# Kernel tuning notes

Measured on AMD Instinct MI355X. Metric: run time of the kernel, lower is better.

Reference implementation:

```python
import jax, jax.numpy as jnp
import numpy as np

B, T, C, H = 2, 2048, 1024, 16
D = C // H
EPS = 1e-5

def _layer_norm(x, w, b):
    mu = jnp.mean(x, axis=-1, keepdims=True)
    var = jnp.var(x, axis=-1, keepdims=True)
    return (x - mu) * jax.lax.rsqrt(var + EPS) * w + b

def setup_inputs() -> dict:
    key = jax.random.key(0)
    ks = jax.random.split(key, 8)
    s = 0.02
    return {
        "x": jax.random.normal(ks[0], (B, T, C), jnp.float32),
        "ln1_w": jnp.ones((C,), jnp.float32),
        "ln1_b": jnp.zeros((C,), jnp.float32),
        "wq": jax.random.normal(ks[1], (C, C), jnp.float32) * s,
        "bq": jnp.zeros((C,), jnp.float32),
        "wk": jax.random.normal(ks[2], (C, C), jnp.float32) * s,
        "bk": jnp.zeros((C,), jnp.float32),
        "wv": jax.random.normal(ks[3], (C, C), jnp.float32) * s,
        "bv": jnp.zeros((C,), jnp.float32),
        "wo": jax.random.normal(ks[4], (C, C), jnp.float32) * s,
        "bo": jnp.zeros((C,), jnp.float32),
        "ln2_w": jnp.ones((C,), jnp.float32),
        "ln2_b": jnp.zeros((C,), jnp.float32),
        "w1": jax.random.normal(ks[5], (C, 4 * C), jnp.float32) * s,
        "b1": jnp.zeros((4 * C,), jnp.float32),
        "w2": jax.random.normal(ks[6], (4 * C, C), jnp.float32) * s,
        "b2": jnp.zeros((C,), jnp.float32),
    }

def reference(x, ln1_w, ln1_b, wq, bq, wk, bk, wv, bv, wo, bo,
              ln2_w, ln2_b, w1, b1, w2, b2):
    # --- attention branch ---
    h = _layer_norm(x, ln1_w, ln1_b)
    q = (h @ wq + bq).reshape(B, T, H, D).transpose(0, 2, 1, 3)  # [B,H,T,D]
    k = (h @ wk + bk).reshape(B, T, H, D).transpose(0, 2, 1, 3)
    v = (h @ wv + bv).reshape(B, T, H, D).transpose(0, 2, 1, 3)
    att = jnp.einsum("bhqd,bhkd->bhqk", q, k) * (1.0 / np.sqrt(D))
    causal = jnp.tril(jnp.ones((T, T), dtype=bool))
    att = jnp.where(causal[None, None], att, jnp.float32(-jnp.inf))
    att = jax.nn.softmax(att, axis=-1)
    y = jnp.einsum("bhqk,bhkd->bhqd", att, v)
    y = y.transpose(0, 2, 1, 3).reshape(B, T, C)
    y = y @ wo + bo
    x = x + y
    # --- MLP branch ---
    h = _layer_norm(x, ln2_w, ln2_b)
    h = jax.nn.gelu(h @ w1 + b1, approximate=False)
    h = h @ w2 + b2
    return x + h
```

## Files before the change

### kernel.cpp

```cpp
#include <hip/hip_runtime.h>
#include <hip/hip_bf16.h>
#include <math.h>

#define B_  2
#define T_  2048
#define C_  1024
#define H_  16
#define D_  64
#define BT_ (B_*T_)

typedef __hip_bfloat16 bf16;
typedef short bf16x8 __attribute__((ext_vector_type(8)));
typedef float floatx4 __attribute__((ext_vector_type(4)));

struct alignas(8) bf4 { bf16 v[4]; };

#define GLOAD_LDS16(g, l) __builtin_amdgcn_global_load_lds(            \
    (const __attribute__((address_space(1))) void*)(g),                \
    (__attribute__((address_space(3))) void*)(l), 16, 0, 0)

__global__ __launch_bounds__(256) void ln_bf16_kernel(const float* __restrict__ x,
    const float* __restrict__ w, const float* __restrict__ b,
    bf16* __restrict__ out)
{
    __shared__ float ps[4], ps2[4];
    __shared__ float sm, srs;
    const int row = blockIdx.x;
    const int tid = threadIdx.x;
    float4 v = ((const float4*)(x + (size_t)row * C_))[tid];
    float s  = v.x + v.y + v.z + v.w;
    float s2 = v.x*v.x + v.y*v.y + v.z*v.z + v.w*v.w;
    for (int off = 32; off > 0; off >>= 1) {
        s  += __shfl_down(s,  off);
        s2 += __shfl_down(s2, off);
    }
    const int wid = tid >> 6;
    if ((tid & 63) == 0) { ps[wid] = s; ps2[wid] = s2; }
    __syncthreads();
    if (tid == 0) {
        float ts  = ps[0] + ps[1] + ps[2] + ps[3];
        float ts2 = ps2[0] + ps2[1] + ps2[2] + ps2[3];
        float mean = ts * (1.0f / C_);
        float var  = ts2 * (1.0f / C_) - mean * mean;
        sm  = mean;
        srs = rsqrtf(var + 1e-5f);
    }
    __syncthreads();
    const float mean = sm, rs = srs;
    float4 wv = ((const float4*)w)[tid];
    float4 bv = ((const float4*)b)[tid];
    bf4 o;
    o.v[0] = __float2bfloat16((v.x - mean) * rs * wv.x + bv.x);
    o.v[1] = __float2bfloat16((v.y - mean) * rs * wv.y + bv.y);
    o.v[2] = __float2bfloat16((v.z - mean) * rs * wv.z + bv.z);
    o.v[3] = __float2bfloat16((v.w - mean) * rs * wv.w + bv.w);
    *(bf4*)(out + (size_t)row * C_ + tid * 4) = o;
}

__device__ __forceinline__ void wconv_body(const float* __restrict__ W,
    bf16* __restrict__ Wt, int K, int N, int k0, int n0)
{
    __shared__ float L[64][65];
    const int t = threadIdx.x;
    const int r = t >> 4, c4 = t & 15;
    #pragma unroll
    for (int p = 0; p < 4; ++p) {
        const int kr = p * 16 + r;
        const float4 v = *(const float4*)(W + (size_t)(k0 + kr) * N + n0 + c4 * 4);
        L[kr][c4*4+0] = v.x; L[kr][c4*4+1] = v.y;
        L[kr][c4*4+2] = v.z; L[kr][c4*4+3] = v.w;
    }
    __syncthreads();
    #pragma unroll
    for (int p = 0; p < 4; ++p) {
        const int nr = p * 16 + r;
        bf4 o;
        o.v[0] = __float2bfloat16(L[c4*4+0][nr]);
        o.v[1] = __float2bfloat16(L[c4*4+1][nr]);
        o.v[2] = __float2bfloat16(L[c4*4+2][nr]);
        o.v[3] = __float2bfloat16(L[c4*4+3][nr]);
        *(bf4*)(Wt + (size_t)(n0 + nr) * K + k0 + c4 * 4) = o;
    }
}

__global__ __launch_bounds__(256) void wconv4_kernel(
    const float* __restrict__ wq, const float* __restrict__ wk,
    const float* __restrict__ wv, const float* __restrict__ wo,
    bf16* __restrict__ wqkvT, bf16* __restrict__ woT)
{
    const int z = blockIdx.z;
    const float* W = (z == 0) ? wq : (z == 1) ? wk : (z == 2) ? wv : wo;
    bf16* Wt = (z == 3) ? woT : wqkvT + (size_t)z * 1024 * 1024;
    wconv_body(W, Wt, 1024, 1024, blockIdx.x * 64, blockIdx.y * 64);
}

__global__ __launch_bounds__(256) void wconv2_kernel(
    const float* __restrict__ w1, const float* __restrict__ w2,
    bf16* __restrict__ w1T, bf16* __restrict__ w2T)
{
    if (blockIdx.z == 0)
        wconv_body(w1, w1T, 1024, 4096, blockIdx.x * 64, blockIdx.y * 64);
    else
        wconv_body(w2, w2T, 4096, 1024, blockIdx.y * 64, blockIdx.x * 64);
}

__global__ void bcat_kernel(const float* __restrict__ bq, const float* __restrict__ bk,
                            const float* __restrict__ bv, float* __restrict__ o)
{
    const int i = blockIdx.x * 256 + threadIdx.x;
    float v = (i < 1024) ? bq[i] : (i < 2048 ? bk[i - 1024] : bv[i - 2048]);
    o[i] = v;
}

__global__ __launch_bounds__(256) void splitk_reduce_kernel(
    float* __restrict__ out, const float* __restrict__ p1,
    const float* __restrict__ bias, const float* __restrict__ res)
{
    const size_t i = (size_t)blockIdx.x * 256 + threadIdx.x;
    float4 o = ((const float4*)out)[i];
    const float4 p = ((const float4*)p1)[i];
    const float4 bb = ((const float4*)bias)[i & (C_ / 4 - 1)];
    const float4 xx = ((const float4*)res)[i];
    o.x += p.x + bb.x + xx.x;
    o.y += p.y + bb.y + xx.y;
    o.z += p.z + bb.z + xx.z;
    o.w += p.w + bb.w + xx.w;
    ((float4*)out)[i] = o;
}

template<int TM, int TN, int BK>
__global__ __launch_bounds__(256) void mfma_gemm_t(
    const bf16* __restrict__ A, const bf16* __restrict__ Wt,
    const float* __restrict__ bias, const float* __restrict__ res,
    void* __restrict__ outv, bf16* __restrict__ vT, float* __restrict__ psplit,
    int M, int N, int K, int ldk, int mode)
{
    constexpr int MI = TM / 32;
    constexpr int NJ = TN / 32;
    constexpr int CPR = BK / 8;
    constexpr int NSLOT = (TM + TN) * CPR / 256;
    __shared__ __align__(16) bf16 smem[(TM + TN) * BK];
    bf16* As = smem;
    bf16* Bs = smem + TM * BK;
    const int tid = threadIdx.x;
    const int w = tid >> 6, l = tid & 63;
    const int fm = l & 15, qd = l >> 4;
    const int m0 = blockIdx.x * TM, n0 = blockIdx.y * TN;
    const int bz = blockIdx.z;
    const int wr = (w >> 1) * (TM / 2), wc = (w & 1) * (TN / 2);

    const bf16* Ab = A  + (size_t)bz * K;
    const bf16* Wb = Wt + (size_t)bz * K;

    const bf16* gsrc[NSLOT];
    bf16* ldst[NSLOT];
    #pragma unroll
    for (int p = 0; p < NSLOT; ++p) {
        const int s = tid + p * 256;
        if (s < TM * CPR) {
            const int row = s / CPR, pos = s % CPR;
            const int ch = pos ^ (row & (CPR - 1));
            gsrc[p] = Ab + (size_t)(m0 + row) * ldk + ch * 8;
            ldst[p] = As + s * 8;
        } else {
            const int s2 = s - TM * CPR;
            const int row = s2 / CPR, pos = s2 % CPR;
            const int ch = pos ^ (row & (CPR - 1));
            gsrc[p] = Wb + (size_t)(n0 + row) * ldk + ch * 8;
            ldst[p] = Bs + s2 * 8;
        }
    }

    floatx4 acc[MI][NJ] = {};

    const int nk = K / BK;
    for (int kk = 0; kk < nk; ++kk) {
        const size_t ko = (size_t)kk * BK;
        __syncthreads();
        #pragma unroll
        for (int p = 0; p < NSLOT; ++p)
            GLOAD_LDS16(gsrc[p] + ko, ldst[p]);
        __syncthreads();
        #pragma unroll
        for (int ks = 0; ks < BK / 32; ++ks) {
            bf16x8 af[MI], bfr[NJ];
            #pragma unroll
            for (int i = 0; i < MI; ++i) {
                const int row = wr + i * 16 + fm;
                af[i] = *(const bf16x8*)(As + row * BK
                        + (((ks * 4 + qd) ^ (row & (CPR - 1))) * 8));
            }
            #pragma unroll
            for (int j = 0; j < NJ; ++j) {
                const int row = wc + j * 16 + fm;
                bfr[j] = *(const bf16x8*)(Bs + row * BK
                        + (((ks * 4 + qd) ^ (row & (CPR - 1))) * 8));
            }
            #pragma unroll
            for (int i = 0; i < MI; ++i)
                #pragma unroll
                for (int j = 0; j < NJ; ++j)
                    acc[i][j] = __builtin_amdgcn_mfma_f32_16x16x32_bf16(
                        af[i], bfr[j], acc[i][j], 0, 0, 0);
        }
    }

    const int col0 = n0 + wc;
    const int row0 = m0 + wr;
    const bool isv = (mode == 3) && (col0 >= 2048);
    const bool bounce = (mode == 0) || (mode == 1) || (mode == 3 && !isv);
    __syncthreads();

    if (bounce) {
        constexpr int RM = TM / 2, RN = TN / 2, CHN = RN / 8;
        bf16* eb = smem + w * (RM * RN);
        #pragma unroll
        for (int j = 0; j < NJ; ++j) {
            const int col = col0 + j * 16 + fm;
            const float bb = bias[col];
            const bool isq = (mode == 3) && (col0 + j * 16 < 1024);
            const int lc = j * 16 + fm;
            #pragma unroll
            for (int i = 0; i < MI; ++i) {
                floatx4 a = acc[i][j];
                #pragma unroll
                for (int r = 0; r < 4; ++r) {
                    float vv = a[r] + bb;
                    if (mode == 1) {
                        float zz = vv * (0.7978845608f + 0.0356774081f * vv * vv);
                        zz = fminf(zz, 15.0f);
                        const float e = __expf(2.0f * zz);
                        vv = vv * (e / (e + 1.0f));
                    }
                    if (isq) vv *= 0.125f;
                    const int lr = i * 16 + qd * 4 + r;
                    const int pch = ((lc >> 3) + 2 * qd) & (CHN - 1);
                    eb[lr * RN + pch * 8 + (lc & 7)] = __float2bfloat16(vv);
                }
            }
        }
        bf16* o = (bf16*)outv;
        #pragma unroll
        for (int c = 0; c < RM * RN / 512; ++c) {
            const int idx = c * 64 + l;
            const int row = idx / CHN;
            const int c8  = idx % CHN;
            const int pch = (c8 + 2 * ((row >> 2) & 3)) & (CHN - 1);
            const bf16x8 vv = *(const bf16x8*)(eb + row * RN + pch * 8);
            *(bf16x8*)(o + (size_t)(row0 + row) * N + col0 + c8 * 8) = vv;
        }
    } else {
        #pragma unroll
        for (int j = 0; j < NJ; ++j) {
            const int col = col0 + j * 16 + fm;
            const float bb = bias[col];
            #pragma unroll
            for (int i = 0; i < MI; ++i) {
                const int row = row0 + i * 16 + qd * 4;
                floatx4 a = acc[i][j];
                if (mode == 4) {
                    float* o = bz ? psplit : (float*)outv;
                    #pragma unroll
                    for (int r = 0; r < 4; ++r)
                        o[(size_t)(row + r) * N + col] = a[r];
                } else if (mode == 2) {
                    float* o = (float*)outv;
                    #pragma unroll
                    for (int r = 0; r < 4; ++r)
                        o[(size_t)(row + r) * N + col] =
                            a[r] + bb + res[(size_t)(row + r) * N + col];
                } else {
                    bf4 pv;
                    #pragma unroll
                    for (int r = 0; r < 4; ++r) pv.v[r] = __float2bfloat16(a[r] + bb);
                    *(bf4*)(vT + (size_t)(col - 2048) * M + row) = pv;
                }
            }
        }
    }
}


#define G8_BARRIER() do {                                   \
    __builtin_amdgcn_sched_barrier(0);                      \
    asm volatile("" ::: "memory");                          \
    __builtin_amdgcn_s_barrier();                           \
    asm volatile("" ::: "memory");                          \
    __builtin_amdgcn_sched_barrier(0);                      \
  } while (0)

#define G8_WAIT_LGKM0() do {                                        \
    asm volatile("s_waitcnt lgkmcnt(0)" ::: "memory");              \
    __builtin_amdgcn_sched_barrier(0);                              \
  } while (0)

#define G8_WAIT_VM(n) asm volatile("s_waitcnt vmcnt(" #n ")" ::: "memory")

#define G8_VW2() do { if (st1) G8_WAIT_VM(8); else G8_WAIT_VM(2); } while (0)
#define G8_VW3() do { if (st1) G8_WAIT_VM(8); else G8_WAIT_VM(0); } while (0)
#define G8_VW1() do { if (st2) G8_WAIT_VM(8); else if (st1) G8_WAIT_VM(4); \
                      else G8_WAIT_VM(0); } while (0)

#define G8_PHASE(Aq, Bq, SC, SG, DB, KO, VW)                                   \
  do {                                                                         \
    const bf16* pa0 = smem + cur * BUF + aof0 + (Aq) * 8192;                   \
    const bf16* pa1 = smem + cur * BUF + aof1 + (Aq) * 8192;                   \
    const bf16* pb0 = smem + cur * BUF + bof0 + (Bq) * 2048;                   \
    const bf16* pb1 = smem + cur * BUF + bof1 + (Bq) * 2048;                   \
    bf16x8 af[4][2], bv[2][2];                                                 \
    _Pragma("unroll")                                                          \
    for (int i = 0; i < 4; ++i) {                                              \
      af[i][0] = *(const bf16x8*)(pa0 + i * 1024);                             \
      af[i][1] = *(const bf16x8*)(pa1 + i * 1024);                             \
    }                                                                          \
    _Pragma("unroll")                                                          \
    for (int jj = 0; jj < 2; ++jj) {                                           \
      bv[jj][0] = *(const bf16x8*)(pb0 + jj * 1024);                           \
      bv[jj][1] = *(const bf16x8*)(pb1 + jj * 1024);                           \
    }                                                                          \
    if (SC) {                                                                  \
      GLOAD_LDS16(gsrc[(SG)*2]     + (KO), smem + (DB) * BUF + lof[(SG)*2]);   \
      GLOAD_LDS16(gsrc[(SG)*2 + 1] + (KO), smem + (DB) * BUF + lof[(SG)*2+1]); \
    }                                                                          \
    G8_BARRIER();                                                              \
    G8_WAIT_LGKM0();                                                           \
    __builtin_amdgcn_s_setprio(1);                                             \
    _Pragma("unroll")                                                          \
    for (int i = 0; i < 4; ++i)                                                \
      _Pragma("unroll")                                                        \
      for (int jj = 0; jj < 2; ++jj) {                                         \
        acc[(Aq)*4+i][(Bq)*2+jj] = __builtin_amdgcn_mfma_f32_16x16x32_bf16(    \
            af[i][0], bv[jj][0], acc[(Aq)*4+i][(Bq)*2+jj], 0, 0, 0);           \
        acc[(Aq)*4+i][(Bq)*2+jj] = __builtin_amdgcn_mfma_f32_16x16x32_bf16(    \
            af[i][1], bv[jj][1], acc[(Aq)*4+i][(Bq)*2+jj], 0, 0, 0);           \
      }                                                                        \
    __builtin_amdgcn_s_setprio(0);                                             \
    VW;                                                                        \
    G8_BARRIER();                                                              \
  } while (0)

template<int MODE>
__global__ __launch_bounds__(512, 2) void gemm8_t(
    const bf16* __restrict__ A, const bf16* __restrict__ Wt,
    const float* __restrict__ bias, bf16* __restrict__ out,
    bf16* __restrict__ vT, int M, int N, int K)
{
    constexpr int BUF = 32768;
    __shared__ __align__(16) bf16 smem[2 * BUF];

    const int tid = threadIdx.x;
    const int w = tid >> 6, l = tid & 63;
    const int fm = l & 15, qd = l >> 4;
    const int wm = w >> 2, wn = w & 3;

    const int nbx = gridDim.x;
    const int nwg = nbx * gridDim.y;
    const int bid = blockIdx.y * nbx + blockIdx.x;
    const int cpx = nwg >> 3;
    const int swz = (bid & 7) * cpx + (bid >> 3);
    const int m0 = (swz % nbx) * 256;
    const int n0 = (swz / nbx) * 256;

    const bf16* gsrc[8];
    int lof[8];
    #pragma unroll
    for (int g = 0; g < 4; ++g) {
        const int isB  = (g & 1);
        const int half = (g >> 1);
        #pragma unroll
        for (int s = 0; s < 2; ++s) {
            const int c = tid + s * 512;
            const int pos = c & 7;
            int row, lofe;
            const bf16* gb;
            if (!isB) {
                row  = half * 128 + (c >> 3);
                gb   = A + (size_t)(m0 + row) * K;
                lofe = row * 64 + pos * 8;
            } else {
                const int vr = c >> 3;
                row  = (vr >> 5) * 64 + half * 32 + (vr & 31);
                gb   = Wt + (size_t)(n0 + row) * K;
                lofe = 16384 + row * 64 + pos * 8;
            }
            const int ch = pos ^ (row & 7);
            gsrc[g * 2 + s] = gb + ch * 8;
            lof[g * 2 + s]  = lofe;
        }
    }

    const int sw0 = qd ^ (fm & 7);
    const int aof0 = (wm * 64 + fm) * 64 + sw0 * 8;
    const int aof1 = (wm * 64 + fm) * 64 + (sw0 ^ 4) * 8;
    const int bof0 = 16384 + (wn * 64 + fm) * 64 + sw0 * 8;
    const int bof1 = 16384 + (wn * 64 + fm) * 64 + (sw0 ^ 4) * 8;

    floatx4 acc[8][4] = {};

    #pragma unroll
    for (int s2 = 0; s2 < 8; ++s2)
        GLOAD_LDS16(gsrc[s2], smem + lof[s2]);
    GLOAD_LDS16(gsrc[2] + 64, smem + BUF + lof[2]);
    GLOAD_LDS16(gsrc[3] + 64, smem + BUF + lof[3]);
    GLOAD_LDS16(gsrc[0] + 64, smem + BUF + lof[0]);
    GLOAD_LDS16(gsrc[1] + 64, smem + BUF + lof[1]);
    G8_WAIT_VM(8);
    G8_BARRIER();

    const int nt = K / 64;
    int cur = 0;
    for (int t = 0; t < nt; ++t, cur ^= 1) {
        const bool st1 = (t + 1 < nt);
        const bool st2 = (t + 2 < nt);
        const int nb = cur ^ 1;
        const size_t ko1 = (size_t)(t + 1) * 64;
        const size_t ko2 = (size_t)(t + 2) * 64;
        G8_PHASE(0, 0, st1, 2, nb,  ko1, G8_VW2());
        G8_PHASE(1, 0, st1, 3, nb,  ko1, G8_VW3());
        G8_PHASE(0, 1, st2, 1, cur, ko2, ;);
        G8_PHASE(1, 1, st2, 0, cur, ko2, G8_VW1());
    }

    G8_WAIT_VM(0);
    G8_BARRIER();

    const int colb = n0 + wn * 64;
    if (MODE == 3 && colb >= 2048) {
        #pragma unroll
        for (int jf = 0; jf < 4; ++jf) {
            const int col = colb + jf * 16 + fm;
            const float bb = bias[col];
            #pragma unroll
            for (int f = 0; f < 8; ++f) {
                const int row = m0 + (f >> 2) * 128 + wm * 64 + (f & 3) * 16 + qd * 4;
                bf4 pv;
                #pragma unroll
                for (int r = 0; r < 4; ++r)
                    pv.v[r] = __float2bfloat16(acc[f][jf][r] + bb);
                *(bf4*)(vT + (size_t)(col - 2048) * M + row) = pv;
            }
        }
    } else {
        const float scale = (MODE == 3 && colb < 1024) ? 0.125f : 1.0f;
        bf16* eb = smem + w * 8192;
        #pragma unroll
        for (int jf = 0; jf < 4; ++jf) {
            const int col = colb + jf * 16 + fm;
            const float bb = bias[col];
            const int lc = jf * 16 + fm;
            const int pch = ((lc >> 3) + 2 * qd) & 7;
            #pragma unroll
            for (int f = 0; f < 8; ++f) {
                const int lr = (f & 3) * 16 + qd * 4;
                #pragma unroll
                for (int r = 0; r < 4; ++r) {
                    float vv = acc[f][jf][r] + bb;
                    if (MODE == 1) {
                        float zz = vv * (0.7978845608f + 0.0356774081f * vv * vv);
                        zz = fminf(zz, 15.0f);
                        const float e = __expf(2.0f * zz);
                        vv = vv * (e / (e + 1.0f));
                    }
                    vv *= scale;
                    eb[(f >> 2) * 4096 + (lr + r) * 64 + pch * 8 + (lc & 7)] =
                        __float2bfloat16(vv);
                }
            }
        }
        #pragma unroll
        for (int p = 0; p < 2; ++p)
            #pragma unroll
            for (int c = 0; c < 8; ++c) {
                const int idx = c * 64 + l;
                const int row = idx >> 3, c8 = idx & 7;
                const int pch = (c8 + 2 * ((row >> 2) & 3)) & 7;
                const bf16x8 vv = *(const bf16x8*)(eb + p * 4096 + row * 64 + pch * 8);
                const int rowg = m0 + p * 128 + wm * 64 + row;
                *(bf16x8*)(out + (size_t)rowg * N + colb + c8 * 8) = vv;
            }
    }
}

__global__ __launch_bounds__(256) void attn_mfma_kernel(
    const bf16* __restrict__ qkv, const bf16* __restrict__ vT,
    bf16* __restrict__ y)
{
    const int pi = blockIdx.x, h = blockIdx.y, b = blockIdx.z;
    const int tid = threadIdx.x, w = tid >> 6, l = tid & 63;
    const int fm = l & 15, qd = l >> 4;
    const int qta = pi, qtb = 31 - pi;
    const float M0 = 3.0f;

    __shared__ __align__(16) bf16 Ks[4096];
    __shared__ __align__(16) bf16 Vs[4096];
    __shared__ __align__(16) bf16 Ps[8][1152];

    const int r0 = tid >> 2,         c0 = (tid & 3) ^ ((r0 >> 1) & 3);
    const int r1 = (tid + 256) >> 2, c1 = ((tid + 256) & 3) ^ ((r1 >> 1) & 3);
    const bf16* kbase = qkv + (size_t)(b * T_) * 3072 + 1024 + h * 64;
    const bf16* vbase = vT + (size_t)(h * 64) * BT_ + b * T_;
    const bf16* kg0 = kbase + (size_t)(r0 & 63) * 3072 + (r0 >> 6) * 32 + c0 * 8;
    const bf16* kg1 = kbase + (size_t)(r1 & 63) * 3072 + (r1 >> 6) * 32 + c1 * 8;
    const bf16* vg0 = vbase + (size_t)(r0 & 63) * BT_ + (r0 >> 6) * 32 + c0 * 8;
    const bf16* vg1 = vbase + (size_t)(r1 & 63) * BT_ + (r1 >> 6) * 32 + c1 * 8;
    bf16* ksl0 = Ks + (size_t)(w * 64) * 8;
    bf16* ksl1 = Ks + (size_t)(w * 64 + 256) * 8;
    bf16* vsl0 = Vs + (size_t)(w * 64) * 8;
    bf16* vsl1 = Vs + (size_t)(w * 64 + 256) * 8;

    const bf16* qpa = qkv + (size_t)(b * T_ + qta * 64 + w * 16 + fm) * 3072 + h * 64 + qd * 8;
    const bf16* qpb = qkv + (size_t)(b * T_ + qtb * 64 + w * 16 + fm) * 3072 + h * 64 + qd * 8;
    const bf16x8 qa0 = *(const bf16x8*)qpa, qa1 = *(const bf16x8*)(qpa + 32);
    const bf16x8 qb0 = *(const bf16x8*)qpb, qb1 = *(const bf16x8*)(qpb + 32);

    const int qba = qta * 64 + w * 16 + qd * 4;
    const int qbb = qtb * 64 + w * 16 + qd * 4;
    const int sw = (qd ^ ((fm >> 1) & 3)) * 8;

    float la[4] = {}, lb[4] = {};
    floatx4 Oa[4] = {}, Ob[4] = {};
    bf16* psa = &Ps[w * 2][0];
    bf16* psb = &Ps[w * 2 + 1][0];

    auto tile = [&](const bf16x8 q0, const bf16x8 q1, float* lsum,
                    floatx4* O, bf16* ps, const int kt, const int qt, const int qb) {
        floatx4 S[4];
        #pragma unroll
        for (int nt = 0; nt < 4; ++nt) {
            const int rr = nt * 16 + fm;
            const bf16x8 k0 = *(const bf16x8*)(Ks + rr * 32 + sw);
            const bf16x8 k1 = *(const bf16x8*)(Ks + (64 + rr) * 32 + sw);
            floatx4 s = {};
            s = __builtin_amdgcn_mfma_f32_16x16x32_bf16(q0, k0, s, 0, 0, 0);
            s = __builtin_amdgcn_mfma_f32_16x16x32_bf16(q1, k1, s, 0, 0, 0);
            S[nt] = s;
        }
        if (kt == qt) {
            #pragma unroll
            for (int nt = 0; nt < 4; ++nt) {
                const int key = kt * 64 + nt * 16 + fm;
                #pragma unroll
                for (int r = 0; r < 4; ++r)
                    if (key > qb + r) S[nt][r] = -1e30f;
            }
        }
        #pragma unroll
        for (int nt = 0; nt < 4; ++nt)
            #pragma unroll
            for (int r = 0; r < 4; ++r) {
                const float p = __expf(S[nt][r] - M0);
                lsum[r] += p;
                ps[(qd * 4 + r) * 72 + nt * 16 + fm] = __float2bfloat16(p);
            }
        #pragma unroll
        for (int s2 = 0; s2 < 2; ++s2) {
            const bf16x8 pf = *(const bf16x8*)(ps + fm * 72 + s2 * 32 + qd * 8);
            #pragma unroll
            for (int nt = 0; nt < 4; ++nt) {
                const bf16x8 vf =
                    *(const bf16x8*)(Vs + (s2 * 64 + nt * 16 + fm) * 32 + sw);
                O[nt] = __builtin_amdgcn_mfma_f32_16x16x32_bf16(pf, vf, O[nt], 0, 0, 0);
            }
        }
    };

    for (int kt = 0; kt <= qtb; ++kt) {
        const size_t kOff = (size_t)kt * 64 * 3072;
        const size_t vOff = (size_t)kt * 64;
        __syncthreads();
        GLOAD_LDS16(kg0 + kOff, ksl0);
        GLOAD_LDS16(kg1 + kOff, ksl1);
        GLOAD_LDS16(vg0 + vOff, vsl0);
        GLOAD_LDS16(vg1 + vOff, vsl1);
        __syncthreads();
        tile(qb0, qb1, lb, Ob, psb, kt, qtb, qbb);
        if (kt <= qta)
            tile(qa0, qa1, la, Oa, psa, kt, qta, qba);
    }

    #pragma unroll
    for (int mk = 1; mk < 16; mk <<= 1)
        #pragma unroll
        for (int r = 0; r < 4; ++r) {
            la[r] += __shfl_xor(la[r], mk);
            lb[r] += __shfl_xor(lb[r], mk);
        }

    #pragma unroll
    for (int r = 0; r < 4; ++r) {
        const float inva = 1.0f / la[r];
        const float invb = 1.0f / lb[r];
        const size_t rowa = (size_t)(b * T_) + qba + r;
        const size_t rowb = (size_t)(b * T_) + qbb + r;
        #pragma unroll
        for (int nt = 0; nt < 4; ++nt) {
            y[rowa * C_ + h * 64 + nt * 16 + fm] = __float2bfloat16(Oa[nt][r] * inva);
            y[rowb * C_ + h * 64 + nt * 16 + fm] = __float2bfloat16(Ob[nt][r] * invb);
        }
    }
}

extern "C" void kernel_launch(void* const* d_in, const int* in_sizes, int n_in,
                              void* d_out, int out_size, void* d_ws, size_t ws_size,
                              hipStream_t stream)
{
    const float* x     = (const float*)d_in[0];
    const float* ln1_w = (const float*)d_in[1];
    const float* ln1_b = (const float*)d_in[2];
    const float* wq    = (const float*)d_in[3];
    const float* bq    = (const float*)d_in[4];
    const float* wk    = (const float*)d_in[5];
    const float* bk    = (const float*)d_in[6];
    const float* wv    = (const float*)d_in[7];
    const float* bv    = (const float*)d_in[8];
    const float* wo    = (const float*)d_in[9];
    const float* bo    = (const float*)d_in[10];
    const float* ln2_w = (const float*)d_in[11];
    const float* ln2_b = (const float*)d_in[12];
    const float* w1    = (const float*)d_in[13];
    const float* b1    = (const float*)d_in[14];
    const float* w2    = (const float*)d_in[15];
    const float* b2    = (const float*)d_in[16];
    float* out = (float*)d_out;

    char* ws = (char*)d_ws;
    const size_t MB = 1024 * 1024;
    bf16*  wqkvT = (bf16*)(ws);
    bf16*  woT   = (bf16*)(ws + 6 * MB);
    bf16*  w1T   = (bf16*)(ws + 8 * MB);
    bf16*  w2T   = (bf16*)(ws + 16 * MB);
    float* bqkv  = (float*)(ws + 24 * MB);
    bf16*  h     = (bf16*)(ws + 24 * MB + 65536);
    bf16*  qkv   = (bf16*)(ws + 32 * MB + 65536);
    bf16*  vT    = (bf16*)(ws + 56 * MB + 65536);
    bf16*  y     = (bf16*)(ws + 64 * MB + 65536);
    float* x2    = (float*)(ws + 72 * MB + 65536);
    bf16*  u     = qkv;
    float* p1    = (float*)ws;

    wconv4_kernel<<<dim3(16, 16, 4), 256, 0, stream>>>(wq, wk, wv, wo, wqkvT, woT);
    wconv2_kernel<<<dim3(16, 64, 2), 256, 0, stream>>>(w1, w2, w1T, w2T);
    bcat_kernel<<<12, 256, 0, stream>>>(bq, bk, bv, bqkv);

    ln_bf16_kernel<<<BT_, 256, 0, stream>>>(x, ln1_w, ln1_b, h);
    gemm8_t<3><<<dim3(16, 12), 512, 0, stream>>>(
        h, wqkvT, bqkv, qkv, vT, BT_, 3072, C_);
    attn_mfma_kernel<<<dim3(16, H_, B_), 256, 0, stream>>>(qkv, vT, y);
    mfma_gemm_t<128, 64, 64><<<dim3(32, 16), 256, 0, stream>>>(
        y, woT, bo, x, x2, nullptr, nullptr, BT_, C_, C_, C_, 2);

    ln_bf16_kernel<<<BT_, 256, 0, stream>>>(x2, ln2_w, ln2_b, h);
    gemm8_t<1><<<dim3(16, 16), 512, 0, stream>>>(
        h, w1T, b1, u, nullptr, BT_, 4 * C_, C_);
    mfma_gemm_t<128, 128, 64><<<dim3(32, 8, 2), 256, 0, stream>>>(
        u, w2T, b2, nullptr, out, nullptr, p1, BT_, C_, 2 * C_, 4 * C_, 4);
    splitk_reduce_kernel<<<BT_ * C_ / 1024, 256, 0, stream>>>(out, p1, b2, x2);
}
```

Baseline: 355.9 us.

## Split GEMM phases by K-half and keep B fragments resident in registers

```diff
diff --git a/kernel.cpp b/kernel.cpp
--- a/kernel.cpp
+++ b/kernel.cpp
@@ -296,27 +296,24 @@
 
 #define G8_WAIT_VM(n) asm volatile("s_waitcnt vmcnt(" #n ")" ::: "memory")
 
-#define G8_VW2() do { if (st1) G8_WAIT_VM(8); else G8_WAIT_VM(2); } while (0)
-#define G8_VW3() do { if (st1) G8_WAIT_VM(8); else G8_WAIT_VM(0); } while (0)
-#define G8_VW1() do { if (st2) G8_WAIT_VM(8); else if (st1) G8_WAIT_VM(4); \
-                      else G8_WAIT_VM(0); } while (0)
-
-#define G8_PHASE(Aq, Bq, SC, SG, DB, KO, VW)                                   \
+#define G8_VW_P0() do { if (s1) G8_WAIT_VM(6); else G8_WAIT_VM(0); } while (0)
+#define G8_VW_P3() do { if (s2) G8_WAIT_VM(6); else if (s1) G8_WAIT_VM(2); \
+                        else G8_WAIT_VM(0); } while (0)
+
+#define G8_PHASE(MH, KS, RB, SC, SG, DB, KO, VW)                               \
   do {                                                                         \
-    const bf16* pa0 = smem + cur * BUF + aof0 + (Aq) * 8192;                   \
-    const bf16* pa1 = smem + cur * BUF + aof1 + (Aq) * 8192;                   \
-    const bf16* pb0 = smem + cur * BUF + bof0 + (Bq) * 2048;                   \
-    const bf16* pb1 = smem + cur * BUF + bof1 + (Bq) * 2048;                   \
-    bf16x8 af[4][2], bv[2][2];                                                 \
+    const bf16* pa = smem + cur * BUF + ((KS) ? aof1 : aof0) + (MH) * 8192;    \
+    bf16x8 af[4];                                                              \
     _Pragma("unroll")                                                          \
-    for (int i = 0; i < 4; ++i) {                                              \
-      af[i][0] = *(const bf16x8*)(pa0 + i * 1024);                             \
-      af[i][1] = *(const bf16x8*)(pa1 + i * 1024);                             \
-    }                                                                          \
-    _Pragma("unroll")                                                          \
-    for (int jj = 0; jj < 2; ++jj) {                                           \
-      bv[jj][0] = *(const bf16x8*)(pb0 + jj * 1024);                           \
-      bv[jj][1] = *(const bf16x8*)(pb1 + jj * 1024);                           \
+    for (int i = 0; i < 4; ++i) af[i] = *(const bf16x8*)(pa + i * 1024);       \
+    if ((RB) == 0) {                                                           \
+      _Pragma("unroll")                                                        \
+      for (int j = 0; j < 4; ++j)                                              \
+        bvr[j][0] = *(const bf16x8*)(smem + cur * BUF + bof0 + j * 1024);      \
+    } else if ((RB) == 1) {                                                    \
+      _Pragma("unroll")                                                        \
+      for (int j = 0; j < 4; ++j)                                              \
+        bvr[j][1] = *(const bf16x8*)(smem + cur * BUF + bof1 + j * 1024);      \
     }                                                                          \
     if (SC) {                                                                  \
       GLOAD_LDS16(gsrc[(SG)*2]     + (KO), smem + (DB) * BUF + lof[(SG)*2]);   \
@@ -328,12 +325,9 @@
     _Pragma("unroll")                                                          \
     for (int i = 0; i < 4; ++i)                                                \
       _Pragma("unroll")                                                        \
-      for (int jj = 0; jj < 2; ++jj) {                                         \
-        acc[(Aq)*4+i][(Bq)*2+jj] = __builtin_amdgcn_mfma_f32_16x16x32_bf16(    \
-            af[i][0], bv[jj][0], acc[(Aq)*4+i][(Bq)*2+jj], 0, 0, 0);           \
-        acc[(Aq)*4+i][(Bq)*2+jj] = __builtin_amdgcn_mfma_f32_16x16x32_bf16(    \
-            af[i][1], bv[jj][1], acc[(Aq)*4+i][(Bq)*2+jj], 0, 0, 0);           \
-      }                                                                        \
+      for (int j = 0; j < 4; ++j)                                              \
+        acc[(MH)*4+i][j] = __builtin_amdgcn_mfma_f32_16x16x32_bf16(            \
+            af[i], bvr[j][KS], acc[(MH)*4+i][j], 0, 0, 0);                     \
     __builtin_amdgcn_s_setprio(0);                                             \
     VW;                                                                        \
     G8_BARRIER();                                                              \
@@ -396,29 +390,35 @@
     const int bof1 = 16384 + (wn * 64 + fm) * 64 + (sw0 ^ 4) * 8;
 
     floatx4 acc[8][4] = {};
-
-    #pragma unroll
-    for (int s2 = 0; s2 < 8; ++s2)
-        GLOAD_LDS16(gsrc[s2], smem + lof[s2]);
+    bf16x8 bvr[4][2];
+
+    GLOAD_LDS16(gsrc[2], smem + lof[2]);
+    GLOAD_LDS16(gsrc[3], smem + lof[3]);
+    GLOAD_LDS16(gsrc[6], smem + lof[6]);
+    GLOAD_LDS16(gsrc[7], smem + lof[7]);
+    GLOAD_LDS16(gsrc[0], smem + lof[0]);
+    GLOAD_LDS16(gsrc[1], smem + lof[1]);
+    GLOAD_LDS16(gsrc[4], smem + lof[4]);
+    GLOAD_LDS16(gsrc[5], smem + lof[5]);
     GLOAD_LDS16(gsrc[2] + 64, smem + BUF + lof[2]);
     GLOAD_LDS16(gsrc[3] + 64, smem + BUF + lof[3]);
-    GLOAD_LDS16(gsrc[0] + 64, smem + BUF + lof[0]);
-    GLOAD_LDS16(gsrc[1] + 64, smem + BUF + lof[1]);
-    G8_WAIT_VM(8);
+    GLOAD_LDS16(gsrc[6] + 64, smem + BUF + lof[6]);
+    GLOAD_LDS16(gsrc[7] + 64, smem + BUF + lof[7]);
+    G8_WAIT_VM(6);
     G8_BARRIER();
 
     const int nt = K / 64;
     int cur = 0;
     for (int t = 0; t < nt; ++t, cur ^= 1) {
-        const bool st1 = (t + 1 < nt);
-        const bool st2 = (t + 2 < nt);
+        const bool s1 = (t + 1 < nt);
+        const bool s2 = (t + 2 < nt);
         const int nb = cur ^ 1;
         const size_t ko1 = (size_t)(t + 1) * 64;
         const size_t ko2 = (size_t)(t + 2) * 64;
-        G8_PHASE(0, 0, st1, 2, nb,  ko1, G8_VW2());
-        G8_PHASE(1, 0, st1, 3, nb,  ko1, G8_VW3());
-        G8_PHASE(0, 1, st2, 1, cur, ko2, ;);
-        G8_PHASE(1, 1, st2, 0, cur, ko2, G8_VW1());
+        G8_PHASE(0, 0,  0, s1, 0, nb,  ko1, G8_VW_P0());
+        G8_PHASE(1, 0,  1, s1, 2, nb,  ko1, ;);
+        G8_PHASE(0, 1, -1, s2, 1, cur, ko2, ;);
+        G8_PHASE(1, 1, -1, s2, 3, cur, ko2, G8_VW_P3());
     }
 
     G8_WAIT_VM(0);
```

Result: no change. 359.6 us (+1.1%).
